# Kernel optimization log

Hardware: AMD Instinct MI355X
Metric: run time of the kernel (lower is better)

## Reference

```python
import jax, jax.numpy as jnp
import numpy as np

N_NODES = 50000
N_EDGES = 800000
GNN_IN, GNN_HID, COMB = 256, 64, 64
MLP_IN, MLP_HID = 256, 512


def glorot(key, shape):
    fan_in, fan_out = shape[0], shape[1]
    s = jnp.sqrt(6.0 / (fan_in + fan_out)).astype(jnp.float32)
    return jax.random.uniform(key, shape, jnp.float32, -s, s)


def setup_inputs() -> dict:
    key = jax.random.key(0)
    ks = jax.random.split(key, 12)
    x = jax.random.normal(ks[0], (N_NODES, GNN_IN), jnp.float32)
    edge_index = jax.random.randint(ks[1], (2, N_EDGES), 0, N_NODES, jnp.int64 if jax.config.jax_enable_x64 else jnp.int32)
    edge_attr = jax.random.uniform(ks[2], (N_EDGES,), jnp.float32)
    user_features = jax.random.normal(ks[3], (N_NODES, MLP_IN), jnp.float32)
    params = {
        'gcn1_W': glorot(ks[4], (GNN_IN, GNN_HID)),
        'gcn1_b': jnp.zeros((GNN_HID,), jnp.float32),
        'gcn2_W': glorot(ks[5], (GNN_HID, COMB)),
        'gcn2_b': jnp.zeros((COMB,), jnp.float32),
        'fc1_W': glorot(ks[6], (MLP_IN, MLP_HID)),
        'fc1_b': jnp.zeros((MLP_HID,), jnp.float32),
        'fc2_W': glorot(ks[7], (MLP_HID, COMB)),
        'fc2_b': jnp.zeros((COMB,), jnp.float32),
        'fcf_W': glorot(ks[8], (2 * COMB, 1)),
        'fcf_b': jnp.zeros((1,), jnp.float32),
    }
    return dict(x=x, edge_index=edge_index, edge_attr=edge_attr,
                user_features=user_features, **params)


def gcn_conv(x, W, b, src, dst, ew, n_nodes):
    # PyG GCNConv: transform, add self-loops (weight 1), sym-normalize, scatter-add.
    h = x @ W  # [N, out]
    loop = jnp.arange(n_nodes, dtype=src.dtype)
    src_sl = jnp.concatenate([src, loop])
    dst_sl = jnp.concatenate([dst, loop])
    ew_sl = jnp.concatenate([ew, jnp.ones((n_nodes,), ew.dtype)])
    deg = jax.ops.segment_sum(ew_sl, dst_sl, num_segments=n_nodes)
    dinv = jnp.where(deg > 0, jax.lax.rsqrt(jnp.maximum(deg, 1e-12)), 0.0)
    norm = dinv[src_sl] * ew_sl * dinv[dst_sl]  # [E+N]
    msg = h[src_sl] * norm[:, None]             # gather + scale
    out = jax.ops.segment_sum(msg, dst_sl, num_segments=n_nodes)
    return out + b


def reference(x, edge_index, edge_attr, user_features,
              gcn1_W, gcn1_b, gcn2_W, gcn2_b,
              fc1_W, fc1_b, fc2_W, fc2_b, fcf_W, fcf_b):
    src, dst = edge_index[0], edge_index[1]
    n = x.shape[0]
    # MLP branch
    mlp_out = jax.nn.relu(user_features @ fc1_W + fc1_b) @ fc2_W + fc2_b
    # GNN branch
    g = gcn_conv(x, gcn1_W, gcn1_b, src, dst, edge_attr, n)
    g = jax.nn.relu(g)
    gnn_out = gcn_conv(g, gcn2_W, gcn2_b, src, dst, edge_attr, n)
    combined = jnp.concatenate([mlp_out, gnn_out], axis=-1)
    return combined @ fcf_W + fcf_b
```

## Files before the change

### kernel.cpp

```cpp
#include <hip/hip_runtime.h>
#include <hip/hip_bf16.h>

#define N_NODES 50000
#define N_EDGES 800000
#define BROW 264
#define NT_TILES 782
#define GRID_H13 512

typedef __attribute__((ext_vector_type(8))) short bfrag8;
typedef __attribute__((ext_vector_type(4))) float f32x4;
typedef __attribute__((ext_vector_type(4))) unsigned short us4;
typedef __attribute__((ext_vector_type(8))) unsigned short us8;

__device__ __forceinline__ float bf2f(unsigned short u) {
  return __uint_as_float(((unsigned int)u) << 16);
}
__device__ __forceinline__ unsigned short f2bf(float f) {
  unsigned int u = __float_as_uint(f);
  u = (u + 0x7fffu + ((u >> 16) & 1u)) >> 16;
  return (unsigned short)u;
}
__device__ __forceinline__ float ldS(const void* p, int f32, size_t i) {
  return f32 ? ((const float*)p)[i] : bf2f(((const unsigned short*)p)[i]);
}
__device__ __forceinline__ void stO(void* out, int f32, int i, float v) {
  if (f32) ((float*)out)[i] = v;
  else ((unsigned short*)out)[i] = f2bf(v);
}

__device__ __forceinline__ void stageLoadBF(const void* src, int nb, us8 st[4]) {
  const int t = threadIdx.x;
  const int r = t & 63, q = t >> 6;
  int row = nb + r; row = row < N_NODES ? row : (N_NODES - 1);
  const us8* s8 = (const us8*)((const unsigned short*)src + (size_t)row * 256 + q * 32);
#pragma unroll
  for (int j = 0; j < 4; ++j) st[j] = s8[j];
}
__device__ __forceinline__ void stageWrite(const us8 st[4], unsigned short* __restrict__ Bs) {
  const int t = threadIdx.x;
  const int r = t & 63, q = t >> 6;
  unsigned short* dst = Bs + r * BROW + q * 32;
#pragma unroll
  for (int j = 0; j < 4; ++j) *(us8*)(dst + j * 8) = st[j];
}
__device__ __forceinline__ void stageF32(const void* src, int nb,
                                         unsigned short* __restrict__ Bs) {
  const int t = threadIdx.x;
  const int r = t & 63, q = t >> 6;
  int row = nb + r; row = row < N_NODES ? row : (N_NODES - 1);
  const f32x4* s4 = (const f32x4*)((const float*)src + (size_t)row * 256 + q * 32);
  unsigned short* dst = Bs + r * BROW + q * 32;
#pragma unroll
  for (int j = 0; j < 4; ++j) {
    f32x4 a = s4[2 * j], b = s4[2 * j + 1];
    us8 o;
    o[0] = f2bf(a[0]); o[1] = f2bf(a[1]); o[2] = f2bf(a[2]); o[3] = f2bf(a[3]);
    o[4] = f2bf(b[0]); o[5] = f2bf(b[1]); o[6] = f2bf(b[2]); o[7] = f2bf(b[3]);
    *(us8*)(dst + j * 8) = o;
  }
}

__global__ void k_detect(const void* x, const void* ea, const void* uf,
                         const void* f1W, const int* ei, int* flags) {
  int lane = threadIdx.x & 63;
  unsigned short ux = ((const unsigned short*)x)[lane];
  unsigned short ue = ((const unsigned short*)ea)[lane];
  unsigned short uu = ((const unsigned short*)uf)[lane];
  unsigned short uw = ((const unsigned short*)f1W)[lane];
  int oi = ei[2 * lane + 1];
  unsigned long long bx = __ballot(((ux >> 7) & 0xFF) > 0x85);
  unsigned long long be = __ballot((ue & 0x8000u) != 0);
  unsigned long long bu = __ballot(((uu >> 7) & 0xFF) > 0x85);
  unsigned long long bw = __ballot(((uw >> 7) & 0xFF) > 0x7E);
  unsigned long long bi = __ballot(oi != 0);
  if (lane == 0) {
    int fx = bx ? 1 : 0, fe = be ? 1 : 0, fu = bu ? 1 : 0, fw = bw ? 1 : 0;
    flags[0] = fx; flags[1] = fe; flags[2] = fu; flags[3] = fw;
    flags[4] = (bi == 0ull) ? 1 : 0;
    flags[5] = (fx & fe & fu & fw);
  }
}

__global__ __launch_bounds__(256) void k_zeroc(int* __restrict__ counts) {
  int i = blockIdx.x * 256 + threadIdx.x;
  if (i <= N_NODES) counts[i] = 0;
}

__global__ __launch_bounds__(256) void k_histpos(const int* __restrict__ ei,
                                                 const int* __restrict__ flags,
                                                 int* __restrict__ counts,
                                                 int* __restrict__ posw) {
  int e = blockIdx.x * 256 + threadIdx.x;
  if (e >= N_EDGES) return;
  int d;
  if (flags[4]) d = ei[1600000 + 2 * e];
  else          d = ei[800000 + e];
  d = d < 0 ? 0 : (d > N_NODES - 1 ? N_NODES - 1 : d);
  posw[e] = atomicAdd(&counts[d], 1);
}

__global__ __launch_bounds__(256) void k_scan1(const int* __restrict__ cnt,
                                               int* __restrict__ rp,
                                               int* __restrict__ bsum) {
  __shared__ int sd[256];
  int t = threadIdx.x;
  int i0 = blockIdx.x * 1024 + t * 4;
  int v0 = (i0 + 0) < N_NODES ? cnt[i0 + 0] : 0;
  int v1 = (i0 + 1) < N_NODES ? cnt[i0 + 1] : 0;
  int v2 = (i0 + 2) < N_NODES ? cnt[i0 + 2] : 0;
  int v3 = (i0 + 3) < N_NODES ? cnt[i0 + 3] : 0;
  int ts = v0 + v1 + v2 + v3;
  sd[t] = ts;
  __syncthreads();
  for (int off = 1; off < 256; off <<= 1) {
    int x = (t >= off) ? sd[t - off] : 0;
    __syncthreads();
    sd[t] += x;
    __syncthreads();
  }
  int exoff = sd[t] - ts;
  if (i0 + 0 < N_NODES) rp[i0 + 0] = exoff;
  if (i0 + 1 < N_NODES) rp[i0 + 1] = exoff + v0;
  if (i0 + 2 < N_NODES) rp[i0 + 2] = exoff + v0 + v1;
  if (i0 + 3 < N_NODES) rp[i0 + 3] = exoff + v0 + v1 + v2;
  if (t == 255) bsum[blockIdx.x] = sd[255];
}

__global__ void k_scan2(const int* __restrict__ bsum, int* __restrict__ boff,
                        int* __restrict__ rp, int nb) {
  if (threadIdx.x == 0) {
    int run = 0;
    for (int b = 0; b < nb; ++b) { boff[b] = run; run += bsum[b]; }
    rp[N_NODES] = run;
  }
}

__global__ __launch_bounds__(256) void k_scan3(int* __restrict__ rp,
                                               const int* __restrict__ boff) {
  int i = blockIdx.x * 256 + threadIdx.x;
  if (i < N_NODES) rp[i] += boff[i >> 10];
}

__global__ __launch_bounds__(256) void k_placeb(const int* __restrict__ ei,
                                                const void* ea,
                                                const int* __restrict__ flags,
                                                const int* __restrict__ rp,
                                                const int* __restrict__ posw,
                                                unsigned long long* __restrict__ e8) {
  int e = blockIdx.x * 256 + threadIdx.x;
  if (e >= N_EDGES) return;
  int s, d;
  if (flags[4]) { s = ei[2 * e]; d = ei[1600000 + 2 * e]; }
  else          { s = ei[e];     d = ei[800000 + e]; }
  s = s < 0 ? 0 : (s > N_NODES - 1 ? N_NODES - 1 : s);
  d = d < 0 ? 0 : (d > N_NODES - 1 ? N_NODES - 1 : d);
  float w = ldS(ea, flags[1], e);
  int pos = rp[d] + posw[e];
  e8[pos] = ((unsigned long long)__float_as_uint(w) << 32) | (unsigned int)s;
}

__global__ __launch_bounds__(256) void k_degc(const int* __restrict__ rp,
                                              const unsigned long long* __restrict__ e8,
                                              float* __restrict__ dinv) {
  const int i = blockIdx.x * 4 + (threadIdx.x >> 6);
  if (i >= N_NODES) return;
  const int lane = threadIdx.x & 63;
  const int base = rp[i], end = rp[i + 1];
  float s = 0.f;
  for (int j = base + lane; j < end; j += 64)
    s += __uint_as_float((unsigned int)(e8[j] >> 32));
#pragma unroll
  for (int off = 32; off > 0; off >>= 1) s += __shfl_xor(s, off, 64);
  if (lane == 0) dinv[i] = rsqrtf(s + 1.0f);
}

__global__ __launch_bounds__(512) void k_prep(
    const void* f1W, const void* g1W, const void* f2W, const void* f2b,
    const void* g2W, const void* g2b, const void* ffW, const void* ffb,
    const int* __restrict__ flags, unsigned short* __restrict__ W1T,
    unsigned short* __restrict__ WgT, float* __restrict__ w2f,
    float* __restrict__ w2g, float* __restrict__ constv) {
  const int fw = flags[3];
  if (blockIdx.x < 288) {
    int tid = blockIdx.x * 512 + threadIdx.x;
    if (tid < 512 * 256) {
      int c = tid >> 8, k = tid & 255;
      W1T[tid] = f2bf(ldS(f1W, fw, (size_t)k * 512 + c));
    } else if (tid < 512 * 256 + 64 * 256) {
      int j = tid - 512 * 256;
      int c = j >> 8, k = j & 255;
      WgT[j] = f2bf(ldS(g1W, fw, (size_t)k * 64 + c));
    }
    return;
  }
  int t = threadIdx.x;
  if (t < 512) {
    float s = 0.f;
    for (int c = 0; c < 64; ++c) s += ldS(f2W, fw, t * 64 + c) * ldS(ffW, fw, c);
    w2f[t] = s;
  }
  if (t < 64) {
    float s = 0.f;
    for (int c = 0; c < 64; ++c) s += ldS(g2W, fw, t * 64 + c) * ldS(ffW, fw, 64 + c);
    w2g[t] = s;
  }
  if (t == 0) {
    float s = ldS(ffb, fw, 0);
    for (int c = 0; c < 64; ++c) {
      s += ldS(f2b, fw, c) * ldS(ffW, fw, c);
      s += ldS(g2b, fw, c) * ldS(ffW, fw, 64 + c);
    }
    constv[0] = s;
  }
}

__global__ __launch_bounds__(512, 2) void k_h13P(
    const void* x, const unsigned short* __restrict__ WgT,
    const float* __restrict__ dinv, const int* __restrict__ flags,
    unsigned short* __restrict__ h1b) {
  __shared__ __align__(16) unsigned short Bs[2][64 * BROW];
  const int f32in = flags[0];
  const int lane = threadIdx.x & 63;
  const int wave = threadIdx.x >> 6;
  const int ct = wave & 3;
  const int nh = wave >> 2;
  const int l15 = lane & 15;
  const int quad = lane >> 4;

  bfrag8 A[8];
  {
    const unsigned short* ap = WgT + (size_t)(ct * 16 + l15) * 256 + quad * 8;
#pragma unroll
    for (int ks = 0; ks < 8; ++ks) A[ks] = *(const bfrag8*)(ap + ks * 32);
  }

  int tile = blockIdx.x;
  if (f32in) stageF32(x, tile * 64, Bs[0]);
  else { us8 st[4]; stageLoadBF(x, tile * 64, st); stageWrite(st, Bs[0]); }
  __syncthreads();

  int cur = 0;
  for (; tile < NT_TILES; tile += GRID_H13) {
    const int nxt = tile + GRID_H13;
    const bool have = nxt < NT_TILES;
    us8 st[4];
    if (!f32in && have) stageLoadBF(x, nxt * 64, st);

    f32x4 acc[2];
    acc[0] = (f32x4){0.f, 0.f, 0.f, 0.f};
    acc[1] = (f32x4){0.f, 0.f, 0.f, 0.f};
    const unsigned short* Bc = Bs[cur];
#pragma unroll
    for (int ks = 0; ks < 8; ++ks) {
      const int bofs = ks * 32 + quad * 8;
#pragma unroll
      for (int u = 0; u < 2; ++u) {
        bfrag8 b = *(const bfrag8*)(Bc + (nh * 32 + u * 16 + l15) * BROW + bofs);
        acc[u] = __builtin_amdgcn_mfma_f32_16x16x32_bf16(A[ks], b, acc[u], 0, 0, 0);
      }
    }

    if (have) {
      if (f32in) stageF32(x, nxt * 64, Bs[cur ^ 1]);
      else       stageWrite(st, Bs[cur ^ 1]);
    }

#pragma unroll
    for (int u = 0; u < 2; ++u) {
      int node = tile * 64 + nh * 32 + u * 16 + l15;
      if (node < N_NODES) {
        float di = dinv[node];
        us4 o;
#pragma unroll
        for (int r = 0; r < 4; ++r) o[r] = f2bf(acc[u][r] * di);
        *(us4*)(h1b + (size_t)node * 64 + ct * 16 + quad * 4) = o;
      }
    }
    __syncthreads();
    cur ^= 1;
  }
}

__global__ __launch_bounds__(512, 2) void k_mlpH(
    const void* uf, const unsigned short* __restrict__ W1T,
    const void* fc1b, const float* __restrict__ w2f,
    const int* __restrict__ flags, float* __restrict__ mlpc,
    float* __restrict__ mlpc2) {
  __shared__ __align__(16) unsigned short Bs[2][64 * BROW];
  __shared__ float red[2][512];
  const int f32in = flags[2];
  const int fw = flags[3];
  const int half = blockIdx.x >> 9;
  const int bid = blockIdx.x & 511;
  const int lane = threadIdx.x & 63;
  const int wave = threadIdx.x >> 6;
  const int l15 = lane & 15;
  const int quad = lane >> 4;
  const int c_base = half * 256 + wave * 32;
  float* __restrict__ mout = half ? mlpc2 : mlpc;

  bfrag8 A[2][8];
  {
    const unsigned short* ap = W1T + (size_t)(c_base + l15) * 256 + quad * 8;
#pragma unroll
    for (int t = 0; t < 2; ++t)
#pragma unroll
      for (int ks = 0; ks < 8; ++ks)
        A[t][ks] = *(const bfrag8*)(ap + (size_t)t * 16 * 256 + ks * 32);
  }

  if (f32in) stageF32(uf, bid * 64, Bs[0]);
  else { us8 st[4]; stageLoadBF(uf, bid * 64, st); stageWrite(st, Bs[0]); }
  __syncthreads();

  int cur = 0, pp = 0;
  for (int tile = bid; tile < NT_TILES; tile += 512) {
    const int nxt = tile + 512;
    const bool have = nxt < NT_TILES;

    f32x4 acc[2][4];
#pragma unroll
    for (int t = 0; t < 2; ++t)
#pragma unroll
      for (int u = 0; u < 4; ++u) acc[t][u] = (f32x4){0.f, 0.f, 0.f, 0.f};

    const unsigned short* Bc = Bs[cur];
#pragma unroll
    for (int ks = 0; ks < 8; ++ks) {
      const int bofs = ks * 32 + quad * 8;
      bfrag8 b[4];
#pragma unroll
      for (int u = 0; u < 4; ++u)
        b[u] = *(const bfrag8*)(Bc + (u * 16 + l15) * BROW + bofs);
#pragma unroll
      for (int t = 0; t < 2; ++t)
#pragma unroll
        for (int u = 0; u < 4; ++u)
          acc[t][u] = __builtin_amdgcn_mfma_f32_16x16x32_bf16(A[t][ks], b[u], acc[t][u], 0, 0, 0);
    }

    float part[4] = {0.f, 0.f, 0.f, 0.f};
#pragma unroll
    for (int t = 0; t < 2; ++t)
#pragma unroll
      for (int r = 0; r < 4; ++r) {
        const int c = c_base + t * 16 + quad * 4 + r;
        const float bc = ldS(fc1b, fw, c);
        const float wc = w2f[c];
#pragma unroll
        for (int u = 0; u < 4; ++u) {
          float v = acc[t][u][r] + bc;
          v = v > 0.f ? v : 0.f;
          part[u] += v * wc;
        }
      }

    if (have) {
      if (f32in) stageF32(uf, nxt * 64, Bs[cur ^ 1]);
      else { us8 st[4]; stageLoadBF(uf, nxt * 64, st); stageWrite(st, Bs[cur ^ 1]); }
    }

#pragma unroll
    for (int u = 0; u < 4; ++u) {
      part[u] += __shfl_xor(part[u], 16, 64);
      part[u] += __shfl_xor(part[u], 32, 64);
      if (lane < 16) red[pp][wave * 64 + u * 16 + l15] = part[u];
    }
    __syncthreads();
    if (threadIdx.x < 64) {
      float sum = 0.f;
#pragma unroll
      for (int w = 0; w < 8; ++w) sum += red[pp][w * 64 + threadIdx.x];
      int node = tile * 64 + threadIdx.x;
      if (node < N_NODES) mout[node] = sum;
    }
    cur ^= 1; pp ^= 1;
  }
}

__global__ __launch_bounds__(256) void k_aggs2(
    const int* __restrict__ rp, const unsigned long long* __restrict__ e8,
    const unsigned short* __restrict__ h1b, const float* __restrict__ dinv,
    const void* g1b, const float* __restrict__ w2g,
    const int* __restrict__ flags, float* __restrict__ s2) {
  const int i = blockIdx.x * 4 + (threadIdx.x >> 6);
  if (i >= N_NODES) return;
  const int lane = threadIdx.x & 63;
  const int base = rp[i], end = rp[i + 1];
  const float di = dinv[i];
  float acc = 0.f;
  int j = base;
  for (; j + 8 <= end; j += 8) {
    unsigned long long vv[8];
#pragma unroll
    for (int q = 0; q < 8; ++q) vv[q] = e8[j + q];
    float ww[8], hv[8];
#pragma unroll
    for (int q = 0; q < 8; ++q) {
      ww[q] = __uint_as_float((unsigned int)(vv[q] >> 32));
      hv[q] = bf2f(h1b[(size_t)(unsigned int)vv[q] * 64 + lane]);
    }
#pragma unroll
    for (int q = 0; q < 8; ++q) acc += ww[q] * hv[q];
  }
  for (; j < end; ++j) {
    unsigned long long v = e8[j];
    acc += __uint_as_float((unsigned int)(v >> 32)) *
           bf2f(h1b[(size_t)(unsigned int)v * 64 + lane]);
  }
  float v = (acc + bf2f(h1b[(size_t)i * 64 + lane])) * di + ldS(g1b, flags[3], lane);
  v = v > 0.f ? v : 0.f;
  float p = v * w2g[lane];
#pragma unroll
  for (int off = 32; off > 0; off >>= 1) p += __shfl_xor(p, off, 64);
  if (lane == 0) s2[i] = di * p;
}

__global__ __launch_bounds__(256) void k_fin2(
    const int* __restrict__ rp, const unsigned long long* __restrict__ e8,
    const float* __restrict__ s2, const float* __restrict__ dinv,
    const float* __restrict__ mlpc, const float* __restrict__ mlpc2,
    const float* __restrict__ constv, const int* __restrict__ flags, void* out) {
  const int i = blockIdx.x * 4 + (threadIdx.x >> 6);
  if (i >= N_NODES) return;
  const int lane = threadIdx.x & 63;
  const int base = rp[i], end = rp[i + 1];
  float p = 0.f;
  for (int j = base + lane; j < end; j += 64) {
    unsigned long long v = e8[j];
    p += __uint_as_float((unsigned int)(v >> 32)) * s2[(unsigned int)v];
  }
#pragma unroll
  for (int off = 32; off > 0; off >>= 1) p += __shfl_xor(p, off, 64);
  if (lane == 0) {
    float di = dinv[i];
    stO(out, flags[5], i, mlpc[i] + mlpc2[i] + di * (p + s2[i]) + constv[0]);
  }
}

__global__ __launch_bounds__(256) void k_zero(const int* __restrict__ flags, void* out) {
  int i = blockIdx.x * 256 + threadIdx.x;
  if (i < N_NODES) stO(out, flags[5], i, 0.f);
}

extern "C" void kernel_launch(void* const* d_in, const int* in_sizes, int n_in,
                              void* d_out, int out_size, void* d_ws, size_t ws_size,
                              hipStream_t stream) {
  const void* x   = d_in[0];
  const int*  ei  = (const int*)d_in[1];
  const void* ea  = d_in[2];
  const void* uf  = d_in[3];
  const void* g1W = d_in[4];
  const void* g1b = d_in[5];
  const void* g2W = d_in[6];
  const void* g2b = d_in[7];
  const void* f1W = d_in[8];
  const void* f1b = d_in[9];
  const void* f2W = d_in[10];
  const void* f2b = d_in[11];
  const void* ffW = d_in[12];
  const void* ffb = d_in[13];

  float* ws = (float*)d_ws;
  int*   flags  = (int*)ws;
  float* w2f    = ws + 16;
  float* w2g    = ws + 528;
  float* constv = ws + 592;
  float* dinv   = ws + 608;
  float* s2     = ws + 50608;
  float* mlpc   = ws + 100608;
  unsigned short* W1T = (unsigned short*)(ws + 150608);
  unsigned short* WgT = W1T + 131072;
  int* rowptr = (int*)(ws + 224336);
  int* bsum   = (int*)(ws + 274352);
  int* boff   = bsum + 64;
  int* counts = (int*)(ws + 274480);
  int* posw   = (int*)(ws + 324496);
  unsigned long long* e8 = (unsigned long long*)(ws + 1124496);
  unsigned short* h1b = (unsigned short*)(ws + 2724496);
  float* mlpc2 = ws + 4324496;
  const size_t NEED = (size_t)4374496 * 4;

  k_detect<<<1, 64, 0, stream>>>(x, ea, uf, f1W, ei, flags);
  if (ws_size < NEED) {
    k_zero<<<(N_NODES + 255) / 256, 256, 0, stream>>>(flags, d_out);
    return;
  }
  const int NZB = (N_NODES + 256) / 256;
  const int NB  = (N_NODES + 1023) / 1024;
  const int NEB = (N_EDGES + 255) / 256;

  k_zeroc<<<NZB, 256, 0, stream>>>(counts);
  k_histpos<<<NEB, 256, 0, stream>>>(ei, flags, counts, posw);
  k_scan1<<<NB, 256, 0, stream>>>(counts, rowptr, bsum);
  k_scan2<<<1, 64, 0, stream>>>(bsum, boff, rowptr, NB);
  k_scan3<<<(N_NODES + 255) / 256, 256, 0, stream>>>(rowptr, boff);
  k_placeb<<<NEB, 256, 0, stream>>>(ei, ea, flags, rowptr, posw, e8);
  k_degc<<<(N_NODES + 3) / 4, 256, 0, stream>>>(rowptr, e8, dinv);
  k_prep<<<289, 512, 0, stream>>>(f1W, g1W, f2W, f2b, g2W, g2b, ffW, ffb, flags,
                                  W1T, WgT, w2f, w2g, constv);
  k_h13P<<<GRID_H13, 512, 0, stream>>>(x, WgT, dinv, flags, h1b);
  k_mlpH<<<1024, 512, 0, stream>>>(uf, W1T, f1b, w2f, flags, mlpc, mlpc2);
  k_aggs2<<<(N_NODES + 3) / 4, 256, 0, stream>>>(rowptr, e8, h1b, dinv, g1b, w2g, flags, s2);
  k_fin2<<<(N_NODES + 3) / 4, 256, 0, stream>>>(rowptr, e8, s2, dinv, mlpc, mlpc2, constv, flags, d_out);
}
```

Before: 359.1 us.

## Replace persistent double-buffered MLP kernel with one block per tile

```diff
diff --git a/kernel.cpp b/kernel.cpp
--- a/kernel.cpp
+++ b/kernel.cpp
@@ -281,17 +281,18 @@
   }
 }
 
-__global__ __launch_bounds__(512, 2) void k_mlpH(
+__global__ __launch_bounds__(512, 2) void k_mlp1(
     const void* uf, const unsigned short* __restrict__ W1T,
     const void* fc1b, const float* __restrict__ w2f,
     const int* __restrict__ flags, float* __restrict__ mlpc,
     float* __restrict__ mlpc2) {
-  __shared__ __align__(16) unsigned short Bs[2][64 * BROW];
-  __shared__ float red[2][512];
+  __shared__ __align__(16) unsigned short Bs[64 * BROW];
+  __shared__ float red[512];
   const int f32in = flags[2];
   const int fw = flags[3];
-  const int half = blockIdx.x >> 9;
-  const int bid = blockIdx.x & 511;
+  int half, tile;
+  if (blockIdx.x < NT_TILES) { half = 0; tile = blockIdx.x; }
+  else                       { half = 1; tile = blockIdx.x - NT_TILES; }
   const int lane = threadIdx.x & 63;
   const int wave = threadIdx.x >> 6;
   const int l15 = lane & 15;
@@ -299,6 +300,9 @@
   const int c_base = half * 256 + wave * 32;
   float* __restrict__ mout = half ? mlpc2 : mlpc;
 
+  us8 stb[4];
+  if (!f32in) stageLoadBF(uf, tile * 64, stb);
+
   bfrag8 A[2][8];
   {
     const unsigned short* ap = W1T + (size_t)(c_base + l15) * 256 + quad * 8;
@@ -309,72 +313,59 @@
         A[t][ks] = *(const bfrag8*)(ap + (size_t)t * 16 * 256 + ks * 32);
   }
 
-  if (f32in) stageF32(uf, bid * 64, Bs[0]);
-  else { us8 st[4]; stageLoadBF(uf, bid * 64, st); stageWrite(st, Bs[0]); }
+  if (f32in) stageF32(uf, tile * 64, Bs);
+  else       stageWrite(stb, Bs);
   __syncthreads();
 
-  int cur = 0, pp = 0;
-  for (int tile = bid; tile < NT_TILES; tile += 512) {
-    const int nxt = tile + 512;
-    const bool have = nxt < NT_TILES;
-
-    f32x4 acc[2][4];
+  f32x4 acc[2][4];
+#pragma unroll
+  for (int t = 0; t < 2; ++t)
+#pragma unroll
+    for (int u = 0; u < 4; ++u) acc[t][u] = (f32x4){0.f, 0.f, 0.f, 0.f};
+
+#pragma unroll
+  for (int ks = 0; ks < 8; ++ks) {
+    const int bofs = ks * 32 + quad * 8;
+    bfrag8 b[4];
+#pragma unroll
+    for (int u = 0; u < 4; ++u)
+      b[u] = *(const bfrag8*)(Bs + (u * 16 + l15) * BROW + bofs);
 #pragma unroll
     for (int t = 0; t < 2; ++t)
 #pragma unroll
-      for (int u = 0; u < 4; ++u) acc[t][u] = (f32x4){0.f, 0.f, 0.f, 0.f};
-
-    const unsigned short* Bc = Bs[cur];
-#pragma unroll
-    for (int ks = 0; ks < 8; ++ks) {
-      const int bofs = ks * 32 + quad * 8;
-      bfrag8 b[4];
-#pragma unroll
       for (int u = 0; u < 4; ++u)
-        b[u] = *(const bfrag8*)(Bc + (u * 16 + l15) * BROW + bofs);
-#pragma unroll
-      for (int t = 0; t < 2; ++t)
-#pragma unroll
-        for (int u = 0; u < 4; ++u)
-          acc[t][u] = __builtin_amdgcn_mfma_f32_16x16x32_bf16(A[t][ks], b[u], acc[t][u], 0, 0, 0);
-    }
-
-    float part[4] = {0.f, 0.f, 0.f, 0.f};
-#pragma unroll
-    for (int t = 0; t < 2; ++t)
-#pragma unroll
-      for (int r = 0; r < 4; ++r) {
-        const int c = c_base + t * 16 + quad * 4 + r;
-        const float bc = ldS(fc1b, fw, c);
-        const float wc = w2f[c];
-#pragma unroll
-        for (int u = 0; u < 4; ++u) {
-          float v = acc[t][u][r] + bc;
-          v = v > 0.f ? v : 0.f;
-          part[u] += v * wc;
-        }
+        acc[t][u] = __builtin_amdgcn_mfma_f32_16x16x32_bf16(A[t][ks], b[u], acc[t][u], 0, 0, 0);
+  }
+
+  float part[4] = {0.f, 0.f, 0.f, 0.f};
+#pragma unroll
+  for (int t = 0; t < 2; ++t)
+#pragma unroll
+    for (int r = 0; r < 4; ++r) {
+      const int c = c_base + t * 16 + quad * 4 + r;
+      const float bc = ldS(fc1b, fw, c);
+      const float wc = w2f[c];
+#pragma unroll
+      for (int u = 0; u < 4; ++u) {
+        float v = acc[t][u][r] + bc;
+        v = v > 0.f ? v : 0.f;
+        part[u] += v * wc;
       }
-
-    if (have) {
-      if (f32in) stageF32(uf, nxt * 64, Bs[cur ^ 1]);
-      else { us8 st[4]; stageLoadBF(uf, nxt * 64, st); stageWrite(st, Bs[cur ^ 1]); }
-    }
-
-#pragma unroll
-    for (int u = 0; u < 4; ++u) {
-      part[u] += __shfl_xor(part[u], 16, 64);
-      part[u] += __shfl_xor(part[u], 32, 64);
-      if (lane < 16) red[pp][wave * 64 + u * 16 + l15] = part[u];
-    }
-    __syncthreads();
-    if (threadIdx.x < 64) {
-      float sum = 0.f;
-#pragma unroll
-      for (int w = 0; w < 8; ++w) sum += red[pp][w * 64 + threadIdx.x];
-      int node = tile * 64 + threadIdx.x;
-      if (node < N_NODES) mout[node] = sum;
-    }
-    cur ^= 1; pp ^= 1;
+    }
+
+#pragma unroll
+  for (int u = 0; u < 4; ++u) {
+    part[u] += __shfl_xor(part[u], 16, 64);
+    part[u] += __shfl_xor(part[u], 32, 64);
+    if (lane < 16) red[wave * 64 + u * 16 + l15] = part[u];
+  }
+  __syncthreads();
+  if (threadIdx.x < 64) {
+    float sum = 0.f;
+#pragma unroll
+    for (int w = 0; w < 8; ++w) sum += red[w * 64 + threadIdx.x];
+    int node = tile * 64 + threadIdx.x;
+    if (node < N_NODES) mout[node] = sum;
   }
 }
 
@@ -500,7 +491,7 @@
   k_prep<<<289, 512, 0, stream>>>(f1W, g1W, f2W, f2b, g2W, g2b, ffW, ffb, flags,
                                   W1T, WgT, w2f, w2g, constv);
   k_h13P<<<GRID_H13, 512, 0, stream>>>(x, WgT, dinv, flags, h1b);
-  k_mlpH<<<1024, 512, 0, stream>>>(uf, W1T, f1b, w2f, flags, mlpc, mlpc2);
+  k_mlp1<<<2 * NT_TILES, 512, 0, stream>>>(uf, W1T, f1b, w2f, flags, mlpc, mlpc2);
   k_aggs2<<<(N_NODES + 3) / 4, 256, 0, stream>>>(rowptr, e8, h1b, dinv, g1b, w2g, flags, s2);
   k_fin2<<<(N_NODES + 3) / 4, 256, 0, stream>>>(rowptr, e8, s2, dinv, mlpc, mlpc2, constv, flags, d_out);
 }
```

New measurement: 354.2 us. About the same (-1.4%).
